# Kernel tuning notes

Hardware: AMD Instinct MI355X
Metric: run time of the kernel (lower is better)

Reference implementation:

```python
import jax, jax.numpy as jnp
import numpy as np

M, K, N = 4096, 4096, 16384  # tokens, input_size, output_size


def setup_inputs() -> dict:
    key = jax.random.key(0)
    k_x, k_w, k_s, k_b = jax.random.split(key, 4)
    x = jax.random.normal(k_x, (M, K), dtype=jnp.float32)
    # Pre-quantized int8 weight, [output_size, input_size] layout as stored by QuantizedLinear.
    weight_q = jax.random.randint(k_w, (N, K), -127, 128, dtype=jnp.int8)
    # Per-channel (per-output) dequant scale; positive, realistic magnitude ~ 2/127.
    weight_scale = (jax.random.uniform(k_s, (N,), dtype=jnp.float32) + 0.5) * (2.0 / 127.0)
    bias = jax.random.normal(k_b, (N,), dtype=jnp.float32)
    return {"x": x, "weight_q": weight_q, "weight_scale": weight_scale, "bias": bias}


def reference(x, weight_q, weight_scale, bias):
    """QuantizedLinear.__call__ with activation_dtype=None, sequence_parallel=False.

    xla_quantized_matmul_local: cast int8 weight to compute dtype, GEMM against x,
    apply per-output-channel weight_scale after the matmul, then add bias.
    weight_q is [N, K]; contraction is x[m,k] * w[n,k] -> out[m,n].
    """
    w = weight_q.astype(jnp.float32)
    out = jnp.einsum("mk,nk->mn", x, w, preferred_element_type=jnp.float32)
    out = out * weight_scale[None, :]  # per-channel dequant
    return out + bias[None, :]
```

## Files before the change

### kernel.cpp

```cpp
#include <hip/hip_runtime.h>

static constexpr int Mdim = 4096;
static constexpr int Kdim = 4096;
static constexpr int Ndim = 16384;
static constexpr int BM = 128, BN = 128, BK = 64;
static constexpr int TILES_N = Ndim / BN;
static constexpr int TILES_M = Mdim / BM;

typedef __attribute__((ext_vector_type(8))) short bf16x8;
typedef __attribute__((ext_vector_type(4))) float f32x4;

__device__ __forceinline__ unsigned packbf(float lo, float hi) {
  unsigned a = __builtin_bit_cast(unsigned, lo);
  unsigned b = __builtin_bit_cast(unsigned, hi);
  a += 0x7FFFu + ((a >> 16) & 1u);
  b += 0x7FFFu + ((b >> 16) & 1u);
  return (a >> 16) | (b & 0xFFFF0000u);
}

__device__ __forceinline__ unsigned i32x2bf(int lo, int hi) {
  float f0 = (float)lo;
  float f1 = (float)hi;
  return (__builtin_bit_cast(unsigned, f0) >> 16) |
         (__builtin_bit_cast(unsigned, f1) & 0xFFFF0000u);
}

__global__ void cvt_x_kernel(const float4* __restrict__ in, uint4* __restrict__ out) {
  int i = blockIdx.x * 256 + threadIdx.x;
  float4 a = in[2 * i];
  float4 b = in[2 * i + 1];
  uint4 o;
  o.x = packbf(a.x, a.y);
  o.y = packbf(a.z, a.w);
  o.z = packbf(b.x, b.y);
  o.w = packbf(b.z, b.w);
  out[i] = o;
}

__global__ void cvt_w_kernel(const int4* __restrict__ in, uint4* __restrict__ out) {
  int i = blockIdx.x * 256 + threadIdx.x;
  int4 a = in[2 * i];
  int4 b = in[2 * i + 1];
  uint4 o;
  o.x = i32x2bf(a.x, a.y);
  o.y = i32x2bf(a.z, a.w);
  o.z = i32x2bf(b.x, b.y);
  o.w = i32x2bf(b.z, b.w);
  out[i] = o;
}

__device__ __forceinline__ void mfma_tile(const unsigned short* As, const unsigned short* Bs,
                                          int am, int bnl, int quad, f32x4 acc[4][4]) {
#pragma unroll
  for (int ks = 0; ks < 2; ++ks) {
    const int c = ks * 4 + quad;
    bf16x8 af[4], bv[4];
#pragma unroll
    for (int t = 0; t < 4; ++t) {
      int ma = am + t * 16;
      af[t] = *(const bf16x8*)(As + (ma * 8 + (c ^ (ma & 7))) * 8);
      int nb = bnl + t * 16;
      bv[t] = *(const bf16x8*)(Bs + (nb * 8 + (c ^ (nb & 7))) * 8);
    }
#pragma unroll
    for (int mi = 0; mi < 4; ++mi)
#pragma unroll
      for (int ni = 0; ni < 4; ++ni)
        acc[mi][ni] = __builtin_amdgcn_mfma_f32_16x16x32_bf16(af[mi], bv[ni], acc[mi][ni], 0, 0, 0);
  }
}

__device__ __forceinline__ void epilogue(float* __restrict__ out,
                                         const float* __restrict__ scale,
                                         const float* __restrict__ bias,
                                         int row0, int col0, int wm, int wn, int lane,
                                         f32x4 acc[4][4]) {
  const int rbase = (lane >> 4) * 4;
#pragma unroll
  for (int ni = 0; ni < 4; ++ni) {
    const int n = col0 + wn * 64 + ni * 16 + (lane & 15);
    const float sc = scale[n];
    const float bz = bias[n];
#pragma unroll
    for (int mi = 0; mi < 4; ++mi) {
      const int m = row0 + wm * 64 + mi * 16 + rbase;
      float* o = out + (long)m * Ndim + n;
#pragma unroll
      for (int r = 0; r < 4; ++r)
        o[(long)r * Ndim] = acc[mi][ni][r] * sc + bz;
    }
  }
}

__global__ __launch_bounds__(256, 2) void gemm_bf16(const unsigned short* __restrict__ A,
                                                    const unsigned short* __restrict__ B,
                                                    const float* __restrict__ scale,
                                                    const float* __restrict__ bias,
                                                    float* __restrict__ out) {
  __shared__ unsigned short As[BM * BK];
  __shared__ unsigned short Bs[BN * BK];

  const int tid = threadIdx.x;
  const int lane = tid & 63;
  const int w = tid >> 6;
  const int wm = w & 1, wn = w >> 1;
  const int bid = blockIdx.x;
  const int bn = bid % TILES_N;
  const int bm = bid / TILES_N;
  const int row0 = bm * BM, col0 = bn * BN;
  const int j4 = w * 4;

  const unsigned short* ag[4];
  const unsigned short* bg[4];
#pragma unroll
  for (int i = 0; i < 4; ++i) {
    int s = (j4 + i) * 64 + lane;
    int m = s >> 3, cs = s & 7, c = cs ^ (m & 7);
    ag[i] = A + (long)(row0 + m) * Kdim + c * 8;
    bg[i] = B + (long)(col0 + m) * Kdim + c * 8;
  }

  f32x4 acc[4][4];
#pragma unroll
  for (int mi = 0; mi < 4; ++mi)
#pragma unroll
    for (int ni = 0; ni < 4; ++ni) acc[mi][ni] = (f32x4){0.f, 0.f, 0.f, 0.f};

  const int am = wm * 64 + (lane & 15);
  const int bnl = wn * 64 + (lane & 15);
  const int quad = lane >> 4;

  for (int kt = 0; kt < Kdim / BK; ++kt) {
    __syncthreads();
#pragma unroll
    for (int i = 0; i < 4; ++i) {
      __builtin_amdgcn_global_load_lds(
          (const __attribute__((address_space(1))) void*)(ag[i] + kt * BK),
          (__attribute__((address_space(3))) void*)(&As[(j4 + i) * 512]), 16, 0, 0);
      __builtin_amdgcn_global_load_lds(
          (const __attribute__((address_space(1))) void*)(bg[i] + kt * BK),
          (__attribute__((address_space(3))) void*)(&Bs[(j4 + i) * 512]), 16, 0, 0);
    }
    __syncthreads();
    mfma_tile(As, Bs, am, bnl, quad, acc);
  }
  epilogue(out, scale, bias, row0, col0, wm, wn, lane, acc);
}

__global__ __launch_bounds__(256, 2) void gemm_fused(const float* __restrict__ X,
                                                     const int* __restrict__ Wq,
                                                     const float* __restrict__ scale,
                                                     const float* __restrict__ bias,
                                                     float* __restrict__ out) {
  __shared__ unsigned short As[BM * BK];
  __shared__ unsigned short Bs[BN * BK];

  const int tid = threadIdx.x;
  const int lane = tid & 63;
  const int w = tid >> 6;
  const int wm = w & 1, wn = w >> 1;
  const int bid = blockIdx.x;
  const int bn = bid % TILES_N;
  const int bm = bid / TILES_N;
  const int row0 = bm * BM, col0 = bn * BN;

  int slot[4];
  long aoff[4], boff[4];
#pragma unroll
  for (int i = 0; i < 4; ++i) {
    int s = i * 256 + tid;
    int m = s >> 3, cs = s & 7, c = cs ^ (m & 7);
    slot[i] = s;
    aoff[i] = (long)(row0 + m) * Kdim + c * 8;
    boff[i] = (long)(col0 + m) * Kdim + c * 8;
  }

  f32x4 acc[4][4];
#pragma unroll
  for (int mi = 0; mi < 4; ++mi)
#pragma unroll
    for (int ni = 0; ni < 4; ++ni) acc[mi][ni] = (f32x4){0.f, 0.f, 0.f, 0.f};

  const int am = wm * 64 + (lane & 15);
  const int bnl = wn * 64 + (lane & 15);
  const int quad = lane >> 4;

  for (int kt = 0; kt < Kdim / BK; ++kt) {
    uint4 aw[4], bw[4];
#pragma unroll
    for (int i = 0; i < 4; ++i) {
      const float4* ap = (const float4*)(X + aoff[i] + kt * BK);
      float4 a0 = ap[0];
      float4 a1 = ap[1];
      aw[i].x = packbf(a0.x, a0.y);
      aw[i].y = packbf(a0.z, a0.w);
      aw[i].z = packbf(a1.x, a1.y);
      aw[i].w = packbf(a1.z, a1.w);
      const int4* bp = (const int4*)(Wq + boff[i] + kt * BK);
      int4 b0 = bp[0];
      int4 b1 = bp[1];
      bw[i].x = i32x2bf(b0.x, b0.y);
      bw[i].y = i32x2bf(b0.z, b0.w);
      bw[i].z = i32x2bf(b1.x, b1.y);
      bw[i].w = i32x2bf(b1.z, b1.w);
    }
    __syncthreads();
#pragma unroll
    for (int i = 0; i < 4; ++i) {
      *(uint4*)(&As[slot[i] * 8]) = aw[i];
      *(uint4*)(&Bs[slot[i] * 8]) = bw[i];
    }
    __syncthreads();
    mfma_tile(As, Bs, am, bnl, quad, acc);
  }
  epilogue(out, scale, bias, row0, col0, wm, wn, lane, acc);
}

extern "C" void kernel_launch(void* const* d_in, const int* in_sizes, int n_in,
                              void* d_out, int out_size, void* d_ws, size_t ws_size,
                              hipStream_t stream) {
  const float* x = (const float*)d_in[0];
  const int* wq = (const int*)d_in[1];
  const float* wscale = (const float*)d_in[2];
  const float* wbias = (const float*)d_in[3];
  float* out = (float*)d_out;

  const size_t needA = ((size_t)Mdim * Kdim + (size_t)Ndim * Kdim) * 2;
  if (ws_size >= needA) {
    unsigned short* xb = (unsigned short*)d_ws;
    unsigned short* wb = xb + (size_t)Mdim * Kdim;
    cvt_x_kernel<<<(Mdim * Kdim) / 8 / 256, 256, 0, stream>>>((const float4*)x, (uint4*)xb);
    cvt_w_kernel<<<(Ndim / 256) * (Kdim / 8), 256, 0, stream>>>((const int4*)wq, (uint4*)wb);
    gemm_bf16<<<TILES_M * TILES_N, 256, 0, stream>>>(xb, wb, wscale, wbias, out);
  } else {
    gemm_fused<<<TILES_M * TILES_N, 256, 0, stream>>>(x, wq, wscale, wbias, out);
  }
}
```

Measured before the change: 998.9 us.

## Replace bf16 GEMM with 256x256 double-buffered 8-phase pipelined kernel

Swaps the 128x128 single-buffered bf16 GEMM for a 256x256-tile kernel with 8 waves, a double-buffered LDS ring fed by direct global-to-LDS loads, and an interleaved schedule. Each K-step is split into four MFMA sub-phases, with staged prefetch loads issued between them. It also uses s_setprio around the MFMA bursts and a workgroup remap across XCDs. The goal is to overlap global memory traffic with compute and raise arithmetic intensity per tile. In exchange it needs more registers and LDS, and hand-placed waitcnt and barrier counts that must stay correct.

```diff
diff --git a/kernel.cpp b/kernel.cpp
--- a/kernel.cpp
+++ b/kernel.cpp
@@ -1,11 +1,19 @@
 #include <hip/hip_runtime.h>
+
 
 static constexpr int Mdim = 4096;
 static constexpr int Kdim = 4096;
 static constexpr int Ndim = 16384;
+
 static constexpr int BM = 128, BN = 128, BK = 64;
 static constexpr int TILES_N = Ndim / BN;
 static constexpr int TILES_M = Mdim / BM;
+
+static constexpr int BM2 = 256, BN2 = 256, BK2 = 64;
+static constexpr int TM2 = Mdim / BM2;
+static constexpr int TN2 = Ndim / BN2;
+static constexpr int NT2 = Kdim / BK2;
+static constexpr int NWG2 = TM2 * TN2;
 
 typedef __attribute__((ext_vector_type(8))) short bf16x8;
 typedef __attribute__((ext_vector_type(4))) float f32x4;
@@ -49,6 +57,201 @@
   out[i] = o;
 }
 
+
+__global__ __launch_bounds__(512, 2) void gemm_bf16_8ph(
+    const unsigned short* __restrict__ A,
+    const unsigned short* __restrict__ B,
+    const float* __restrict__ scale,
+    const float* __restrict__ bias,
+    float* __restrict__ out) {
+  __shared__ unsigned short As[2 * 2 * 1024 * 8];
+  __shared__ unsigned short Bs[2 * 2 * 1024 * 8];
+
+  const int tid = threadIdx.x;
+  const int lane = tid & 63;
+  const int w = tid >> 6;
+  const int wm = w >> 2;
+  const int wn = w & 3;
+  const int l15 = lane & 15;
+  const int quad = lane >> 4;
+  const int sw = l15 & 7;
+  const int bhalf = wn >> 1;
+
+  const int bid = blockIdx.x;
+  const int wg = (bid & 7) * (NWG2 / 8) + (bid >> 3);
+  const int bm = wg / TN2, bn = wg % TN2;
+  const int row0 = bm * BM2, col0 = bn * BN2;
+
+  unsigned aoff[2][2], boff[2][2];
+#pragma unroll
+  for (int h = 0; h < 2; ++h)
+#pragma unroll
+    for (int i = 0; i < 2; ++i) {
+      int ch = (w * 2 + i) * 64 + lane;
+      int ir = ch >> 3;
+      int c = (ch & 7) ^ (ir & 7);
+      int ra = (ir >> 6) * 128 + h * 64 + (ir & 63);
+      int rb = h * 128 + ir;
+      aoff[h][i] = (unsigned)((((long)(row0 + ra)) * Kdim + c * 8) * 2);
+      boff[h][i] = (unsigned)((((long)(col0 + rb)) * Kdim + c * 8) * 2);
+    }
+
+#define STG_A(d, h, kt)                                                                   \
+  do {                                                                                    \
+    __builtin_amdgcn_global_load_lds(                                                     \
+        (const __attribute__((address_space(1))) void*)((const char*)A + aoff[h][0] + (kt)*128), \
+        (__attribute__((address_space(3))) void*)(&As[(((d)*2 + (h)) * 1024 + (w*2 + 0) * 64) * 8]), 16, 0, 0); \
+    __builtin_amdgcn_global_load_lds(                                                     \
+        (const __attribute__((address_space(1))) void*)((const char*)A + aoff[h][1] + (kt)*128), \
+        (__attribute__((address_space(3))) void*)(&As[(((d)*2 + (h)) * 1024 + (w*2 + 1) * 64) * 8]), 16, 0, 0); \
+  } while (0)
+
+#define STG_B(d, h, kt)                                                                   \
+  do {                                                                                    \
+    __builtin_amdgcn_global_load_lds(                                                     \
+        (const __attribute__((address_space(1))) void*)((const char*)B + boff[h][0] + (kt)*128), \
+        (__attribute__((address_space(3))) void*)(&Bs[(((d)*2 + (h)) * 1024 + (w*2 + 0) * 64) * 8]), 16, 0, 0); \
+    __builtin_amdgcn_global_load_lds(                                                     \
+        (const __attribute__((address_space(1))) void*)((const char*)B + boff[h][1] + (kt)*128), \
+        (__attribute__((address_space(3))) void*)(&Bs[(((d)*2 + (h)) * 1024 + (w*2 + 1) * 64) * 8]), 16, 0, 0); \
+  } while (0)
+
+#define LDA(dst, d, h, t3, ks)                                                            \
+  dst = *(const bf16x8*)(As + ((((d)*2 + (h)) * 1024 + (wm * 64 + (t3) * 16 + l15) * 8 +  \
+                                (((ks)*4 + quad) ^ sw)) * 8))
+#define LDB(dst, d, n, ks)                                                                \
+  dst = *(const bf16x8*)(Bs + ((((d)*2 + bhalf) * 1024 + ((wn & 1) * 64 + (n) * 16 + l15) * 8 + \
+                                (((ks)*4 + quad) ^ sw)) * 8))
+
+  f32x4 acc[8][4];
+#pragma unroll
+  for (int mi = 0; mi < 8; ++mi)
+#pragma unroll
+    for (int ni = 0; ni < 4; ++ni) acc[mi][ni] = (f32x4){0.f, 0.f, 0.f, 0.f};
+
+  bf16x8 af[4][2];
+  bf16x8 bf[4][2];
+
+  auto GROUP = [&](int g, int d, bool s1, bool s2) {
+    const int dn = d ^ 1;
+#pragma unroll
+    for (int t = 0; t < 4; ++t) {
+      LDA(af[t][0], d, 0, t, 0);
+      LDA(af[t][1], d, 0, t, 1);
+    }
+#pragma unroll
+    for (int n = 0; n < 2; ++n) {
+      LDB(bf[n][0], d, n, 0);
+      LDB(bf[n][1], d, n, 1);
+    }
+    if (s1) STG_A(dn, 1, g + 1);
+    __builtin_amdgcn_s_barrier();
+    asm volatile("s_waitcnt lgkmcnt(0)" ::: "memory");
+    __builtin_amdgcn_s_setprio(1);
+#pragma unroll
+    for (int mi = 0; mi < 4; ++mi)
+#pragma unroll
+      for (int ni = 0; ni < 2; ++ni)
+#pragma unroll
+        for (int ks = 0; ks < 2; ++ks)
+          acc[mi][ni] = __builtin_amdgcn_mfma_f32_16x16x32_bf16(af[mi][ks], bf[ni][ks], acc[mi][ni], 0, 0, 0);
+    __builtin_amdgcn_s_setprio(0);
+    __builtin_amdgcn_s_barrier();
+
+#pragma unroll
+    for (int n = 0; n < 2; ++n) {
+      LDB(bf[2 + n][0], d, 2 + n, 0);
+      LDB(bf[2 + n][1], d, 2 + n, 1);
+    }
+    if (s2) STG_A(d, 0, g + 2);
+    __builtin_amdgcn_s_barrier();
+    asm volatile("s_waitcnt lgkmcnt(0)" ::: "memory");
+    __builtin_amdgcn_s_setprio(1);
+#pragma unroll
+    for (int mi = 0; mi < 4; ++mi)
+#pragma unroll
+      for (int ni = 0; ni < 2; ++ni)
+#pragma unroll
+        for (int ks = 0; ks < 2; ++ks)
+          acc[mi][2 + ni] = __builtin_amdgcn_mfma_f32_16x16x32_bf16(af[mi][ks], bf[2 + ni][ks], acc[mi][2 + ni], 0, 0, 0);
+    __builtin_amdgcn_s_setprio(0);
+    __builtin_amdgcn_s_barrier();
+
+#pragma unroll
+    for (int t = 0; t < 4; ++t) {
+      LDA(af[t][0], d, 1, t, 0);
+      LDA(af[t][1], d, 1, t, 1);
+    }
+    if (s2) STG_B(d, 0, g + 2);
+    __builtin_amdgcn_s_barrier();
+    asm volatile("s_waitcnt lgkmcnt(0)" ::: "memory");
+    __builtin_amdgcn_s_setprio(1);
+#pragma unroll
+    for (int mi = 0; mi < 4; ++mi)
+#pragma unroll
+      for (int ni = 0; ni < 2; ++ni)
+#pragma unroll
+        for (int ks = 0; ks < 2; ++ks)
+          acc[4 + mi][ni] = __builtin_amdgcn_mfma_f32_16x16x32_bf16(af[mi][ks], bf[ni][ks], acc[4 + mi][ni], 0, 0, 0);
+    __builtin_amdgcn_s_setprio(0);
+    __builtin_amdgcn_s_barrier();
+
+    if (s2) STG_B(d, 1, g + 2);
+    __builtin_amdgcn_s_barrier();
+    __builtin_amdgcn_s_setprio(1);
+#pragma unroll
+    for (int mi = 0; mi < 4; ++mi)
+#pragma unroll
+      for (int ni = 0; ni < 2; ++ni)
+#pragma unroll
+        for (int ks = 0; ks < 2; ++ks)
+          acc[4 + mi][2 + ni] = __builtin_amdgcn_mfma_f32_16x16x32_bf16(af[mi][ks], bf[2 + ni][ks], acc[4 + mi][2 + ni], 0, 0, 0);
+    __builtin_amdgcn_s_setprio(0);
+    asm volatile("s_waitcnt vmcnt(6)" ::: "memory");
+    __builtin_amdgcn_s_barrier();
+  };
+
+  STG_A(0, 0, 0);
+  STG_A(0, 1, 0);
+  STG_B(0, 0, 0);
+  STG_B(0, 1, 0);
+  STG_A(1, 0, 1);
+  STG_B(1, 0, 1);
+  STG_B(1, 1, 1);
+  asm volatile("s_waitcnt vmcnt(6)" ::: "memory");
+  __builtin_amdgcn_s_barrier();
+
+#pragma unroll 1
+  for (int g = 0; g < NT2 - 2; g += 2) {
+    GROUP(g, 0, true, true);
+    GROUP(g + 1, 1, true, true);
+  }
+  GROUP(NT2 - 2, 0, true, false);
+  asm volatile("s_waitcnt vmcnt(0)" ::: "memory");
+  __builtin_amdgcn_s_barrier();
+  GROUP(NT2 - 1, 1, false, false);
+
+#undef STG_A
+#undef STG_B
+#undef LDA
+#undef LDB
+
+  const int rbase = quad * 4;
+#pragma unroll
+  for (int ni = 0; ni < 4; ++ni) {
+    const int n = col0 + wn * 64 + ni * 16 + l15;
+    const float sc = scale[n];
+    const float bz = bias[n];
+#pragma unroll
+    for (int mi = 0; mi < 8; ++mi) {
+      const int m = row0 + wm * 128 + mi * 16 + rbase;
+      float* o = out + (long)m * Ndim + n;
+#pragma unroll
+      for (int r = 0; r < 4; ++r) o[(long)r * Ndim] = acc[mi][ni][r] * sc + bz;
+    }
+  }
+}
+
 __device__ __forceinline__ void mfma_tile(const unsigned short* As, const unsigned short* Bs,
                                           int am, int bnl, int quad, f32x4 acc[4][4]) {
 #pragma unroll
@@ -70,11 +273,11 @@
   }
 }
 
-__device__ __forceinline__ void epilogue(float* __restrict__ out,
-                                         const float* __restrict__ scale,
-                                         const float* __restrict__ bias,
-                                         int row0, int col0, int wm, int wn, int lane,
-                                         f32x4 acc[4][4]) {
+__device__ __forceinline__ void epilogue128(float* __restrict__ out,
+                                            const float* __restrict__ scale,
+                                            const float* __restrict__ bias,
+                                            int row0, int col0, int wm, int wn, int lane,
+                                            f32x4 acc[4][4]) {
   const int rbase = (lane >> 4) * 4;
 #pragma unroll
   for (int ni = 0; ni < 4; ++ni) {
@@ -90,61 +293,6 @@
         o[(long)r * Ndim] = acc[mi][ni][r] * sc + bz;
     }
   }
-}
-
-__global__ __launch_bounds__(256, 2) void gemm_bf16(const unsigned short* __restrict__ A,
-                                                    const unsigned short* __restrict__ B,
-                                                    const float* __restrict__ scale,
-                                                    const float* __restrict__ bias,
-                                                    float* __restrict__ out) {
-  __shared__ unsigned short As[BM * BK];
-  __shared__ unsigned short Bs[BN * BK];
-
-  const int tid = threadIdx.x;
-  const int lane = tid & 63;
-  const int w = tid >> 6;
-  const int wm = w & 1, wn = w >> 1;
-  const int bid = blockIdx.x;
-  const int bn = bid % TILES_N;
-  const int bm = bid / TILES_N;
-  const int row0 = bm * BM, col0 = bn * BN;
-  const int j4 = w * 4;
-
-  const unsigned short* ag[4];
-  const unsigned short* bg[4];
-#pragma unroll
-  for (int i = 0; i < 4; ++i) {
-    int s = (j4 + i) * 64 + lane;
-    int m = s >> 3, cs = s & 7, c = cs ^ (m & 7);
-    ag[i] = A + (long)(row0 + m) * Kdim + c * 8;
-    bg[i] = B + (long)(col0 + m) * Kdim + c * 8;
-  }
-
-  f32x4 acc[4][4];
-#pragma unroll
-  for (int mi = 0; mi < 4; ++mi)
-#pragma unroll
-    for (int ni = 0; ni < 4; ++ni) acc[mi][ni] = (f32x4){0.f, 0.f, 0.f, 0.f};
-
-  const int am = wm * 64 + (lane & 15);
-  const int bnl = wn * 64 + (lane & 15);
-  const int quad = lane >> 4;
-
-  for (int kt = 0; kt < Kdim / BK; ++kt) {
-    __syncthreads();
-#pragma unroll
-    for (int i = 0; i < 4; ++i) {
-      __builtin_amdgcn_global_load_lds(
-          (const __attribute__((address_space(1))) void*)(ag[i] + kt * BK),
-          (__attribute__((address_space(3))) void*)(&As[(j4 + i) * 512]), 16, 0, 0);
-      __builtin_amdgcn_global_load_lds(
-          (const __attribute__((address_space(1))) void*)(bg[i] + kt * BK),
-          (__attribute__((address_space(3))) void*)(&Bs[(j4 + i) * 512]), 16, 0, 0);
-    }
-    __syncthreads();
-    mfma_tile(As, Bs, am, bnl, quad, acc);
-  }
-  epilogue(out, scale, bias, row0, col0, wm, wn, lane, acc);
 }
 
 __global__ __launch_bounds__(256, 2) void gemm_fused(const float* __restrict__ X,
@@ -213,7 +361,7 @@
     __syncthreads();
     mfma_tile(As, Bs, am, bnl, quad, acc);
   }
-  epilogue(out, scale, bias, row0, col0, wm, wn, lane, acc);
+  epilogue128(out, scale, bias, row0, col0, wm, wn, lane, acc);
 }
 
 extern "C" void kernel_launch(void* const* d_in, const int* in_sizes, int n_in,
@@ -231,7 +379,7 @@
     unsigned short* wb = xb + (size_t)Mdim * Kdim;
     cvt_x_kernel<<<(Mdim * Kdim) / 8 / 256, 256, 0, stream>>>((const float4*)x, (uint4*)xb);
     cvt_w_kernel<<<(Ndim / 256) * (Kdim / 8), 256, 0, stream>>>((const int4*)wq, (uint4*)wb);
-    gemm_bf16<<<TILES_M * TILES_N, 256, 0, stream>>>(xb, wb, wscale, wbias, out);
+    gemm_bf16_8ph<<<NWG2, 512, 0, stream>>>(xb, wb, wscale, wbias, out);
   } else {
     gemm_fused<<<TILES_M * TILES_N, 256, 0, stream>>>(x, wq, wscale, wbias, out);
   }
```

Measured after the change: 1.626 ms. 62.8% more time.
